# Kernel tuning notes

Measured on AMD Instinct MI355X. Metric: run time of the kernel, lower is better.

The kernel has to match this reference:

```python
import jax, jax.numpy as jnp
import numpy as np

B, N, DIM = 4, 1024, 2048
H, HKV, D = 16, 4, 128          # n_heads, n_kv_heads, head_dim
CACHE = 3072                     # cached KV length
WINDOW = 2048                    # max_window_len (sliding window)
EPS = 1e-6


def setup_inputs() -> dict:
    key = jax.random.key(0)
    ks = jax.random.split(key, 10)
    x = jax.random.normal(ks[0], (B, N, DIM), dtype=jnp.float32)
    past_k = jax.random.normal(ks[1], (B, HKV, CACHE, D), dtype=jnp.float32)
    past_v = jax.random.normal(ks[2], (B, HKV, CACHE, D), dtype=jnp.float32)
    # RoPE angles for the current segment (absolute positions CACHE..CACHE+N-1),
    # matching MultiLevelRoPE 'face' level: freqs = 1/theta**(arange(0,D,2)/D)
    pos = jnp.arange(CACHE, CACHE + N, dtype=jnp.float32)
    inv_freq = 1.0 / (10000.0 ** (jnp.arange(0, D, 2, dtype=jnp.float32) / D))
    ang = pos[:, None] * inv_freq[None, :]          # [N, D//2]
    freqs_cos = jnp.cos(ang)
    freqs_sin = jnp.sin(ang)
    s = 0.02
    Wq = jax.random.normal(ks[3], (H * D, DIM), dtype=jnp.float32) * s
    Wk = jax.random.normal(ks[4], (HKV * D, DIM), dtype=jnp.float32) * s
    Wv = jax.random.normal(ks[5], (HKV * D, DIM), dtype=jnp.float32) * s
    Wo = jax.random.normal(ks[6], (DIM, H * D), dtype=jnp.float32) * s
    bo = jnp.zeros((DIM,), dtype=jnp.float32)
    wq_norm = jnp.ones((D,), dtype=jnp.float32)
    wk_norm = jnp.ones((D,), dtype=jnp.float32)
    return {"x": x, "past_k": past_k, "past_v": past_v,
            "freqs_cos": freqs_cos, "freqs_sin": freqs_sin,
            "Wq": Wq, "Wk": Wk, "Wv": Wv, "Wo": Wo, "bo": bo,
            "wq_norm": wq_norm, "wk_norm": wk_norm}


def _rms_norm(t, w):
    # torch.nn.RMSNorm over head_dim
    return t * jax.lax.rsqrt(jnp.mean(t * t, axis=-1, keepdims=True) + EPS) * w


def _rope(t, cos, sin):
    # interleaved-pair complex rotation, as in MultiLevelRoPE.apply
    # t: [B, h, N, D]; cos/sin: [N, D//2]
    t2 = t.reshape(*t.shape[:-1], D // 2, 2)
    x0, x1 = t2[..., 0], t2[..., 1]
    c = cos[None, None, :, :]
    s = sin[None, None, :, :]
    r0 = x0 * c - x1 * s
    r1 = x0 * s + x1 * c
    return jnp.stack([r0, r1], axis=-1).reshape(t.shape)


def reference(x, past_k, past_v, freqs_cos, freqs_sin,
              Wq, Wk, Wv, Wo, bo, wq_norm, wk_norm):
    # projections -> [B, h, N, D]
    q = (x @ Wq.T).reshape(B, N, H, D).transpose(0, 2, 1, 3)
    k = (x @ Wk.T).reshape(B, N, HKV, D).transpose(0, 2, 1, 3)
    v = (x @ Wv.T).reshape(B, N, HKV, D).transpose(0, 2, 1, 3)
    # qk rms_norm on head_dim
    q = _rms_norm(q, wq_norm)
    k = _rms_norm(k, wk_norm)
    # RoPE on current segment (cached K already rotated)
    q = _rope(q, freqs_cos, freqs_sin)
    k = _rope(k, freqs_cos, freqs_sin)
    # append to cache -> M = CACHE + N
    k_all = jnp.concatenate([past_k, k], axis=2)   # [B, HKV, M, D]
    v_all = jnp.concatenate([past_v, v], axis=2)
    # repeat_kv for GQA
    n_rep = H // HKV
    k_rep = jnp.repeat(k_all, n_rep, axis=1)       # [B, H, M, D]
    v_rep = jnp.repeat(v_all, n_rep, axis=1)
    M = CACHE + N
    scale = 1.0 / jnp.sqrt(jnp.asarray(D, dtype=q.dtype))
    scores = jnp.einsum('bhnd,bhmd->bhnm', q, k_rep) * scale
    # causal + sliding-window mask over absolute positions
    qpos = jnp.arange(N) + CACHE                   # [N]
    kpos = jnp.arange(M)                           # [M]
    allowed = (kpos[None, :] <= qpos[:, None]) & (qpos[:, None] - kpos[None, :] < WINDOW)
    scores = jnp.where(allowed[None, None], scores, jnp.asarray(-1e30, dtype=scores.dtype))
    probs = jax.nn.softmax(scores, axis=-1)
    attn = jnp.einsum('bhnm,bhmd->bhnd', probs, v_rep)
    attn = attn.transpose(0, 2, 1, 3).reshape(B, N, H * D)
    return attn @ Wo.T + bo
```

## Files before the change

kernel.cpp:

```cpp
#include <hip/hip_runtime.h>
#include <hip/hip_bf16.h>
#include <stdint.h>

typedef unsigned short u16;
typedef unsigned int u32;
typedef __attribute__((ext_vector_type(8))) __bf16 bfrag;
typedef __attribute__((ext_vector_type(4))) float f32x4;
typedef __attribute__((ext_vector_type(16))) float f32x16;
typedef __attribute__((ext_vector_type(4))) unsigned short u16x4;

__device__ __forceinline__ u16 f2bf(float f){
  union { float f; u32 u; } v; v.f = f;
  u32 u = v.u;
  return (u16)((u + 0x7fffu + ((u >> 16) & 1u)) >> 16);
}

__device__ __forceinline__ u32 cvtpk(float a, float b){
  u32 r; asm("v_cvt_pk_bf16_f32 %0, %1, %2" : "=v"(r) : "v"(a), "v"(b)); return r;
}
__device__ __forceinline__ void swap32(u32 &a, u32 &b){
  asm volatile("v_permlane32_swap_b32 %0, %1" : "+v"(a), "+v"(b));
}

__device__ __forceinline__ void gload_lds16(const void* g, void* l){
  __builtin_amdgcn_global_load_lds(
      (__attribute__((address_space(1))) void*)(unsigned long long)g,
      (__attribute__((address_space(3))) void*)(u32)(unsigned long long)l,
      16, 0, 0);
}

__global__ void __launch_bounds__(256) k_cvt(const float* __restrict__ s, u16* __restrict__ d, int n4){
  int i = blockIdx.x*256 + threadIdx.x;
  if (i >= n4) return;
  float4 v = ((const float4*)s)[i];
  u16x4 o; o[0]=f2bf(v.x); o[1]=f2bf(v.y); o[2]=f2bf(v.z); o[3]=f2bf(v.w);
  ((u16x4*)d)[i] = o;
}

__global__ void __launch_bounds__(256) k_past_kr(const float* __restrict__ pk, u16* __restrict__ Kr){
  __shared__ u16 TK[64][128];
  const int kc = 16 + blockIdx.x;
  const int pl = blockIdx.y;
  const int t = threadIdx.x;
  const float* src = pk + (size_t)pl*393216 + (size_t)kc*8192;
  #pragma unroll
  for (int i = 0; i < 8; ++i){
    int e = i*1024 + t*4;
    float4 v = *(const float4*)(src + e);
    u16x4 o; o[0]=f2bf(v.x); o[1]=f2bf(v.y); o[2]=f2bf(v.z); o[3]=f2bf(v.w);
    *(u16x4*)&TK[e>>7][e&127] = o;
  }
  __syncthreads();
  u16* dst = Kr + (size_t)pl*524288 + (size_t)kc*8192;
  #pragma unroll
  for (int i = 0; i < 4; ++i){
    int f = i*256 + t;
    int fhi = f >> 6, lf = f & 63;
    int row = ((f >> 9) << 5) | (lf & 31);
    int col = ((fhi & 7) << 4) | ((lf >> 5) << 3);
    bfrag v = *(const bfrag*)&TK[row][col];
    *(bfrag*)(dst + fhi*512 + lf*8) = v;
  }
}

__global__ void __launch_bounds__(256) k_past_vr(const float* __restrict__ pv, u16* __restrict__ Vr){
  __shared__ u16 T2[128][80];
  const int kc = 16 + blockIdx.x;
  const int pl = blockIdx.y;
  const int t = threadIdx.x;
  const float* src = pv + (size_t)pl*393216 + (size_t)kc*8192;
  #pragma unroll
  for (int i = 0; i < 8; ++i){
    int e = i*1024 + t*4;
    int row = e >> 7, d0 = e & 127;
    float4 v = *(const float4*)(src + e);
    T2[d0][row]   = f2bf(v.x);
    T2[d0+1][row] = f2bf(v.y);
    T2[d0+2][row] = f2bf(v.z);
    T2[d0+3][row] = f2bf(v.w);
  }
  __syncthreads();
  u16* dst = Vr + (size_t)pl*524288 + (size_t)kc*8192;
  #pragma unroll
  for (int i = 0; i < 4; ++i){
    int g = i*256 + t;
    int ghi = g >> 6, lg = g & 63;
    int d  = ((ghi & 3) << 5) | (lg & 31);
    int k0 = ((g >> 9) << 5) | (((ghi >> 2) & 1) << 4) | ((lg >> 5) << 3);
    bfrag v = *(const bfrag*)&T2[d][k0];
    *(bfrag*)(dst + ghi*512 + lg*8) = v;
  }
}

__global__ void __launch_bounds__(256) k_new_vr(const u16* __restrict__ vn, u16* __restrict__ Vr){
  __shared__ u16 T2[128][80];
  const int kcl = blockIdx.x;
  const int pl = blockIdx.y;
  const int t = threadIdx.x;
  const u16* src = vn + (size_t)pl*131072 + (size_t)kcl*8192;
  #pragma unroll
  for (int i = 0; i < 4; ++i){
    int e = i*2048 + t*8;
    int row = e >> 7, d0 = e & 127;
    union { bfrag v; u16 x[8]; } u;
    u.v = *(const bfrag*)(src + e);
    #pragma unroll
    for (int j = 0; j < 8; ++j) T2[d0+j][row] = u.x[j];
  }
  __syncthreads();
  u16* dst = Vr + (size_t)pl*524288 + (size_t)(48 + kcl)*8192;
  #pragma unroll
  for (int i = 0; i < 4; ++i){
    int g = i*256 + t;
    int ghi = g >> 6, lg = g & 63;
    int d  = ((ghi & 3) << 5) | (lg & 31);
    int k0 = ((g >> 9) << 5) | (((ghi >> 2) & 1) << 4) | ((lg >> 5) << 3);
    bfrag v = *(const bfrag*)&T2[d][k0];
    *(bfrag*)(dst + ghi*512 + lg*8) = v;
  }
}

template<int EPI>
__global__ void __launch_bounds__(256) k_gemm(
    const u16* __restrict__ A, const u16* __restrict__ Bm,
    u16* __restrict__ Cb, float* __restrict__ Cf, const float* __restrict__ bias,
    int M, int Nn, int K)
{
  __shared__ u16 lsA[2][4096];
  __shared__ u16 lsB[2][4096];
  const int t = threadIdx.x, lane = t & 63, wid = t >> 6;
  const int l15 = lane & 15, l4 = lane >> 4;
  const int wm = wid >> 1, wn = wid & 1;
  const int bn = blockIdx.x, bm = blockIdx.y;
  const u16* Ab = A + (size_t)bm*128*K;
  const u16* Bb = Bm + (size_t)bn*128*K;

  auto stage = [&](u16* ls, const u16* g, int kof){
    #pragma unroll
    for (int r = 0; r < 2; ++r){
      int row = r*64 + (t >> 2);
      int s = (t & 3) ^ ((row >> 1) & 3);
      gload_lds16(g + (size_t)row*K + kof + s*8, ls + r*2048 + wid*512);
    }
  };

  f32x4 acc[4][4] = {};
  stage(&lsA[0][0], Ab, 0);
  stage(&lsB[0][0], Bb, 0);
  const int NT = K >> 5;
  const int sl = l4 ^ ((l15 >> 1) & 3);
  const int ra0 = wm*64 + l15, rb0 = wn*64 + l15;
  for (int kt = 0; kt < NT; ++kt){
    __syncthreads();
    const int cur = kt & 1;
    if (kt + 1 < NT){
      stage(&lsA[cur ^ 1][0], Ab, (kt + 1)*32);
      stage(&lsB[cur ^ 1][0], Bb, (kt + 1)*32);
    }
    bfrag af[4], bfv[4];
    #pragma unroll
    for (int i = 0; i < 4; ++i){
      af[i]  = *(const bfrag*)&lsA[cur][(ra0 + i*16)*32 + sl*8];
      bfv[i] = *(const bfrag*)&lsB[cur][(rb0 + i*16)*32 + sl*8];
    }
    #pragma unroll
    for (int i = 0; i < 4; ++i)
      #pragma unroll
      for (int j = 0; j < 4; ++j)
        acc[i][j] = __builtin_amdgcn_mfma_f32_16x16x32_bf16(af[i], bfv[j], acc[i][j], 0, 0, 0);
  }
  const int row0 = bm*128 + wm*64, col0 = bn*128 + wn*64;
  #pragma unroll
  for (int i = 0; i < 4; ++i)
    #pragma unroll
    for (int j = 0; j < 4; ++j){
      int cc = col0 + j*16 + l15;
      float bv = (EPI == 1) ? bias[cc] : 0.f;
      #pragma unroll
      for (int r = 0; r < 4; ++r){
        int rr = row0 + i*16 + l4*4 + r;
        if (EPI == 0) Cb[(size_t)rr*Nn + cc] = f2bf(acc[i][j][r]);
        else          Cf[(size_t)rr*Nn + cc] = acc[i][j][r] + bv;
      }
    }
}

__global__ void __launch_bounds__(256) k_rmsrope(
    const u16* __restrict__ proj, const float* __restrict__ cosb, const float* __restrict__ sinb,
    const float* __restrict__ wq, const float* __restrict__ wk,
    u16* __restrict__ q_ro, u16* __restrict__ Kr, u16* __restrict__ v_new)
{
  const int bn = blockIdx.x;
  const int b = bn >> 10, n = bn & 1023;
  const int lane = threadIdx.x & 63, w = threadIdx.x >> 6;
  const int chunk = blockIdx.y*4 + w;
  const u16* src = proj + (size_t)bn*3072 + chunk*128 + lane*2;
  const u32 raw = *(const u32*)src;
  union { u32 u; float f; } a, c2;
  a.u = raw << 16; c2.u = raw & 0xffff0000u;
  float x0 = a.f, x1 = c2.f;
  if (chunk >= 20){
    int hk = chunk - 20;
    *(u32*)(v_new + ((size_t)(b*4 + hk)*1024 + n)*128 + lane*2) = raw;
    return;
  }
  float ss = x0*x0 + x1*x1;
  #pragma unroll
  for (int m = 1; m < 64; m <<= 1) ss += __shfl_xor(ss, m, 64);
  float inv = rsqrtf(ss*(1.f/128.f) + 1e-6f);
  const float* wn2 = (chunk < 16) ? wq : wk;
  x0 *= inv*wn2[lane*2]; x1 *= inv*wn2[lane*2 + 1];
  float cz = cosb[n*64 + lane], sz = sinb[n*64 + lane];
  float r0 = x0*cz - x1*sz;
  float r1 = x0*sz + x1*cz;
  if (chunk < 16){
    const float KLF = 0.127529904f;
    r0 *= KLF; r1 *= KLF;
    u32 outp = (u32)f2bf(r0) | ((u32)f2bf(r1) << 16);
    *(u32*)(q_ro + (((size_t)(b*16 + chunk)*1024 + n) << 7) + lane*2) = outp;
  } else {
    int hk = chunk - 16;
    u32 outp = (u32)f2bf(r0) | ((u32)f2bf(r1) << 16);
    int kpos = 3072 + n;
    size_t idx = (size_t)(b*4 + hk)*524288
               + (size_t)(((kpos >> 6)*16) + (((kpos >> 5) & 1)*8) + (lane >> 3))*512
               + (size_t)((((lane >> 2) & 1) << 5) | (kpos & 31))*8
               + ((2*lane) & 7);
    *(u32*)(Kr + idx) = outp;
  }
}

__global__ void __launch_bounds__(512, 2) k_attn(
    const u16* __restrict__ q_ro, const u16* __restrict__ Kr,
    const u16* __restrict__ Vr, u16* __restrict__ attn_o)
{
  __shared__ u16 smem[32768];
  __shared__ float Lsh[4][32];
  const int bid = blockIdx.x;
  const int xcd = bid & 7, idx = bid >> 3;
  const int plane = (xcd << 1) | (idx >> 5);
  const int qt = idx & 31;
  const int b = plane >> 2, hk = plane & 3;
  const int t = threadIdx.x, lane = t & 63, w = t >> 6;
  const int l31 = lane & 31, lh = lane >> 5;
  const int hf = w >> 2;
  const int hd = w & 3;
  const int h = hk*4 + hd;
  const int qbase = qt*32;

  const u16* qplane = q_ro + (size_t)(b*16 + h)*1024*128;
  const u16* kplane = Kr + (size_t)(b*4 + hk)*524288;
  const u16* vplane = Vr + (size_t)(b*4 + hk)*524288;

  bfrag qf[8];
  {
    const u16* qrow = qplane + (size_t)(qbase + l31)*128 + lh*8;
    #pragma unroll
    for (int dks = 0; dks < 8; ++dks)
      qf[dks] = *(const bfrag*)(qrow + dks*16);
  }

  const int kb0 = (qbase + 1024) & ~63;
  const int kc0 = kb0 >> 6;
  const int qpos = 3072 + qbase + l31;

  const char* smb = (const char*)smem;
  const int krd = hf*8192 + lane*16;
  const int vrd = 32768 + hf*8192 + lane*16;

  auto stageK = [&](int c2, int buf){
    const u16* ks = kplane + (size_t)(kc0 + c2)*8192 + t*8;
    gload_lds16(ks,        smem + buf*8192 + t*8);
    gload_lds16(ks + 4096, smem + buf*8192 + 4096 + t*8);
  };
  auto stageV = [&](int c2, int buf){
    const u16* vs = vplane + (size_t)(kc0 + c2)*8192 + t*8;
    gload_lds16(vs,        smem + 16384 + buf*8192 + t*8);
    gload_lds16(vs + 4096, smem + 16384 + buf*8192 + 4096 + t*8);
  };

  f32x16 acc_o[4] = {};
  float l_run = 0.f;

  stageK(0, 0); stageK(1, 1); stageV(0, 0);
  __syncthreads();

  f32x16 sA, sB;
  {
    #pragma unroll
    for (int r = 0; r < 16; ++r) sA[r] = 0.f;
    __builtin_amdgcn_s_setprio(1);
    #pragma unroll
    for (int dks = 0; dks < 8; ++dks){
      bfrag kf = *(const bfrag*)(smb + krd + dks*1024);
      sA = __builtin_amdgcn_mfma_f32_32x32x16_bf16(kf, qf[dks], sA, 0, 0, 0);
    }
    __builtin_amdgcn_s_setprio(0);
  }

  auto body = [&](int c, f32x16& sCur, f32x16& sNxt){
    __syncthreads();
    if (c <= 30) stageK(c + 2, c & 1);
    if (c <= 31) stageV(c + 1, (c + 1) & 1);

    if (c < 32){
      #pragma unroll
      for (int r = 0; r < 16; ++r) sNxt[r] = 0.f;
      const int kbase = krd + ((c + 1) & 1)*16384;
      __builtin_amdgcn_s_setprio(1);
      #pragma unroll
      for (int dks = 0; dks < 8; ++dks){
        bfrag kf = *(const bfrag*)(smb + kbase + dks*1024);
        sNxt = __builtin_amdgcn_mfma_f32_32x32x16_bf16(kf, qf[dks], sNxt, 0, 0, 0);
      }
      __builtin_amdgcn_s_setprio(0);
    }

    bfrag vf[8];
    const int vbase = vrd + (c & 1)*16384;
    #pragma unroll
    for (int g = 0; g < 8; ++g) vf[g] = *(const bfrag*)(smb + vbase + g*1024);

    if ((c == 0) | (c == 32)){
      const int kb = kb0 + c*64;
      #pragma unroll
      for (int r = 0; r < 16; ++r){
        int kpos = kb + hf*32 + (r & 3) + 8*(r >> 2) + 4*lh;
        int dq = qpos - kpos;
        if ((unsigned)dq >= 2048u) sCur[r] = -1e30f;
      }
    }

    #pragma unroll
    for (int r = 0; r < 16; ++r) sCur[r] = exp2f(sCur[r]);
    {
      float a0 = (sCur[0]+sCur[1]) + (sCur[2]+sCur[3]);
      float a1 = (sCur[4]+sCur[5]) + (sCur[6]+sCur[7]);
      float a2 = (sCur[8]+sCur[9]) + (sCur[10]+sCur[11]);
      float a3 = (sCur[12]+sCur[13]) + (sCur[14]+sCur[15]);
      float lc = (a0 + a1) + (a2 + a3);
      lc += __shfl_xor(lc, 32, 64);
      l_run += lc;
    }

    union { u32 u[4]; bfrag v; } pf[2];
    {
      u32 a0 = cvtpk(sCur[0],  sCur[1]),  a1 = cvtpk(sCur[2],  sCur[3]);
      u32 b0 = cvtpk(sCur[4],  sCur[5]),  b1 = cvtpk(sCur[6],  sCur[7]);
      swap32(a0, b0); swap32(a1, b1);
      pf[0].u[0]=a0; pf[0].u[1]=a1; pf[0].u[2]=b0; pf[0].u[3]=b1;
      u32 c0 = cvtpk(sCur[8],  sCur[9]),  c1 = cvtpk(sCur[10], sCur[11]);
      u32 e0 = cvtpk(sCur[12], sCur[13]), e1 = cvtpk(sCur[14], sCur[15]);
      swap32(c0, e0); swap32(c1, e1);
      pf[1].u[0]=c0; pf[1].u[1]=c1; pf[1].u[2]=e0; pf[1].u[3]=e1;
    }

    __builtin_amdgcn_s_setprio(1);
    #pragma unroll
    for (int lks = 0; lks < 2; ++lks)
      #pragma unroll
      for (int dj = 0; dj < 4; ++dj)
        acc_o[dj] = __builtin_amdgcn_mfma_f32_32x32x16_bf16(vf[lks*4 + dj], pf[lks].v, acc_o[dj], 0, 0, 0);
    __builtin_amdgcn_s_setprio(0);
  };

  #pragma unroll 1
  for (int cc = 0; cc < 16; ++cc){
    body(2*cc,     sA, sB);
    body(2*cc + 1, sB, sA);
  }
  body(32, sA, sB);

  #pragma unroll
  for (int p = 0; p < 2; ++p){
    __syncthreads();
    if (hf == 1 && (hd >> 1) == p){
      if (lh == 0) Lsh[hd][l31] = l_run;
      float* om = (float*)smem + (hd & 1)*4096;
      #pragma unroll
      for (int dj = 0; dj < 4; ++dj)
        #pragma unroll
        for (int rg = 0; rg < 4; ++rg){
          int slot = dj*8 + rg*2 + lh;
          f32x4 vv;
          #pragma unroll
          for (int j = 0; j < 4; ++j) vv[j] = acc_o[dj][rg*4 + j];
          *(f32x4*)&om[l31*128 + ((slot ^ (l31 & 7)) << 2)] = vv;
        }
    }
    __syncthreads();
    if (hf == 0 && (hd >> 1) == p){
      const float* om = (const float*)smem + (hd & 1)*4096;
      float ltot = l_run + Lsh[hd][l31];
      float inv = 1.0f / ltot;
      const int bn = b*1024 + qbase + l31;
      u16* orow = attn_o + (size_t)bn*2048 + h*128;
      #pragma unroll
      for (int dj = 0; dj < 4; ++dj)
        #pragma unroll
        for (int rg = 0; rg < 4; ++rg){
          int slot = dj*8 + rg*2 + lh;
          f32x4 vv = *(const f32x4*)&om[l31*128 + ((slot ^ (l31 & 7)) << 2)];
          int d0 = dj*32 + rg*8 + lh*4;
          u16x4 o;
          #pragma unroll
          for (int j = 0; j < 4; ++j) o[j] = f2bf((acc_o[dj][rg*4 + j] + vv[j])*inv);
          *(u16x4*)(orow + d0) = o;
        }
    }
  }
}

extern "C" void kernel_launch(void* const* d_in, const int* in_sizes, int n_in,
                              void* d_out, int out_size, void* d_ws, size_t ws_size,
                              hipStream_t stream)
{
  const float* x      = (const float*)d_in[0];
  const float* past_k = (const float*)d_in[1];
  const float* past_v = (const float*)d_in[2];
  const float* fcos   = (const float*)d_in[3];
  const float* fsin   = (const float*)d_in[4];
  const float* Wq     = (const float*)d_in[5];
  const float* Wk     = (const float*)d_in[6];
  const float* Wv     = (const float*)d_in[7];
  const float* Wo     = (const float*)d_in[8];
  const float* bo     = (const float*)d_in[9];
  const float* wqn    = (const float*)d_in[10];
  const float* wkn    = (const float*)d_in[11];
  float* out = (float*)d_out;
  char* ws = (char*)d_ws;

  u16* xb    = (u16*)(ws);
  u16* wqkv  = (u16*)(ws + 16777216);
  u16* wo_b  = (u16*)(ws + 29360128);
  u16* q_ro  = (u16*)(ws + 37748736);
  u16* Kr    = (u16*)(ws + 54525952);
  u16* Vr    = (u16*)(ws + 71303168);
  u16* v_new = (u16*)(ws + 88080384);
  u16* proj  = (u16*)(ws + 92274688);
  u16* attn_o = proj;

  k_cvt<<<8192, 256, 0, stream>>>(x, xb, 2097152);
  k_cvt<<<4096, 256, 0, stream>>>(Wq, wqkv, 1048576);
  k_cvt<<<1024, 256, 0, stream>>>(Wk, wqkv + 2048*2048, 262144);
  k_cvt<<<1024, 256, 0, stream>>>(Wv, wqkv + 2560*2048, 262144);
  k_cvt<<<4096, 256, 0, stream>>>(Wo, wo_b, 1048576);
  k_past_kr<<<dim3(32, 16), 256, 0, stream>>>(past_k, Kr);
  k_past_vr<<<dim3(32, 16), 256, 0, stream>>>(past_v, Vr);

  k_gemm<0><<<dim3(24, 32), 256, 0, stream>>>(xb, wqkv, proj, nullptr, nullptr, 4096, 3072, 2048);
  k_rmsrope<<<dim3(4096, 6), 256, 0, stream>>>(proj, fcos, fsin, wqn, wkn, q_ro, Kr, v_new);
  k_new_vr<<<dim3(16, 16), 256, 0, stream>>>(v_new, Vr);
  k_attn<<<512, 512, 0, stream>>>(q_ro, Kr, Vr, attn_o);
  k_gemm<1><<<dim3(16, 32), 256, 0, stream>>>(attn_o, wo_b, nullptr, out, bo, 4096, 2048, 2048);
}
```

Measured before the change: 255.4 us.

## Pre-swizzle GEMM operands into MFMA fragment layout and enlarge GEMM tiles

```diff
diff --git a/kernel.cpp b/kernel.cpp
--- a/kernel.cpp
+++ b/kernel.cpp
@@ -29,12 +29,18 @@
       16, 0, 0);
 }
 
-__global__ void __launch_bounds__(256) k_cvt(const float* __restrict__ s, u16* __restrict__ d, int n4){
+__global__ void __launch_bounds__(256) k_cvt_frag(const float* __restrict__ s, u16* __restrict__ d,
+                                                  int n4, int NF, int n_off){
   int i = blockIdx.x*256 + threadIdx.x;
   if (i >= n4) return;
+  int e = i*4;
+  int ln = e >> 11, k = e & 2047;
+  int n = n_off + ln;
   float4 v = ((const float4*)s)[i];
   u16x4 o; o[0]=f2bf(v.x); o[1]=f2bf(v.y); o[2]=f2bf(v.z); o[3]=f2bf(v.w);
-  ((u16x4*)d)[i] = o;
+  size_t idx = ((size_t)((k >> 5)*NF + (n >> 4)))*512
+             + (size_t)(((n & 15) | (((k >> 3) & 3) << 4)))*8 + (k & 4);
+  *(u16x4*)(d + idx) = o;
 }
 
 __global__ void __launch_bounds__(256) k_past_kr(const float* __restrict__ pk, u16* __restrict__ Kr){
@@ -121,59 +127,50 @@
 }
 
 template<int EPI>
-__global__ void __launch_bounds__(256) k_gemm(
-    const u16* __restrict__ A, const u16* __restrict__ Bm,
-    u16* __restrict__ Cb, float* __restrict__ Cf, const float* __restrict__ bias,
-    int M, int Nn, int K)
+__global__ void __launch_bounds__(512, 2) k_gemm(
+    const u16* __restrict__ Af, const u16* __restrict__ Bf,
+    u16* __restrict__ Cb, float* __restrict__ Cf, const float* __restrict__ bias, int Nn)
 {
-  __shared__ u16 lsA[2][4096];
+  __shared__ u16 lsA[2][8192];
   __shared__ u16 lsB[2][4096];
-  const int t = threadIdx.x, lane = t & 63, wid = t >> 6;
+  const int t = threadIdx.x, lane = t & 63;
   const int l15 = lane & 15, l4 = lane >> 4;
-  const int wm = wid >> 1, wn = wid & 1;
+  const int w = t >> 6, wm = w >> 2, wn = w & 3;
   const int bn = blockIdx.x, bm = blockIdx.y;
-  const u16* Ab = A + (size_t)bm*128*K;
-  const u16* Bb = Bm + (size_t)bn*128*K;
-
-  auto stage = [&](u16* ls, const u16* g, int kof){
-    #pragma unroll
-    for (int r = 0; r < 2; ++r){
-      int row = r*64 + (t >> 2);
-      int s = (t & 3) ^ ((row >> 1) & 3);
-      gload_lds16(g + (size_t)row*K + kof + s*8, ls + r*2048 + wid*512);
-    }
-  };
-
-  f32x4 acc[4][4] = {};
-  stage(&lsA[0][0], Ab, 0);
-  stage(&lsB[0][0], Bb, 0);
-  const int NT = K >> 5;
-  const int sl = l4 ^ ((l15 >> 1) & 3);
-  const int ra0 = wm*64 + l15, rb0 = wn*64 + l15;
-  for (int kt = 0; kt < NT; ++kt){
+  const int NF = Nn >> 4;
+  const u16* As = Af + (size_t)(bm*16)*512 + t*8;
+
+  f32x4 acc[8][2] = {};
+  gload_lds16(As,        &lsA[0][t*8]);
+  gload_lds16(As + 4096, &lsA[0][4096 + t*8]);
+  gload_lds16(Bf + ((size_t)bn*8)*512 + t*8, &lsB[0][t*8]);
+
+  for (int kt = 0; kt < 64; ++kt){
     __syncthreads();
     const int cur = kt & 1;
-    if (kt + 1 < NT){
-      stage(&lsA[cur ^ 1][0], Ab, (kt + 1)*32);
-      stage(&lsB[cur ^ 1][0], Bb, (kt + 1)*32);
-    }
-    bfrag af[4], bfv[4];
-    #pragma unroll
-    for (int i = 0; i < 4; ++i){
-      af[i]  = *(const bfrag*)&lsA[cur][(ra0 + i*16)*32 + sl*8];
-      bfv[i] = *(const bfrag*)&lsB[cur][(rb0 + i*16)*32 + sl*8];
-    }
-    #pragma unroll
-    for (int i = 0; i < 4; ++i)
-      #pragma unroll
-      for (int j = 0; j < 4; ++j)
-        acc[i][j] = __builtin_amdgcn_mfma_f32_16x16x32_bf16(af[i], bfv[j], acc[i][j], 0, 0, 0);
-  }
-  const int row0 = bm*128 + wm*64, col0 = bn*128 + wn*64;
-  #pragma unroll
-  for (int i = 0; i < 4; ++i)
-    #pragma unroll
-    for (int j = 0; j < 4; ++j){
+    if (kt < 63){
+      const u16* An = As + (size_t)(kt + 1)*131072;
+      const u16* Bn = Bf + ((size_t)(kt + 1)*NF + bn*8)*512 + t*8;
+      gload_lds16(An,        &lsA[cur ^ 1][t*8]);
+      gload_lds16(An + 4096, &lsA[cur ^ 1][4096 + t*8]);
+      gload_lds16(Bn,        &lsB[cur ^ 1][t*8]);
+    }
+    bfrag bf2[2];
+    #pragma unroll
+    for (int j = 0; j < 2; ++j)
+      bf2[j] = *(const bfrag*)&lsB[cur][(wn*2 + j)*512 + lane*8];
+    #pragma unroll
+    for (int i = 0; i < 8; ++i){
+      bfrag af = *(const bfrag*)&lsA[cur][(wm*8 + i)*512 + lane*8];
+      acc[i][0] = __builtin_amdgcn_mfma_f32_16x16x32_bf16(af, bf2[0], acc[i][0], 0, 0, 0);
+      acc[i][1] = __builtin_amdgcn_mfma_f32_16x16x32_bf16(af, bf2[1], acc[i][1], 0, 0, 0);
+    }
+  }
+  const int row0 = bm*256 + wm*128, col0 = bn*128 + wn*32;
+  #pragma unroll
+  for (int i = 0; i < 8; ++i)
+    #pragma unroll
+    for (int j = 0; j < 2; ++j){
       int cc = col0 + j*16 + l15;
       float bv = (EPI == 1) ? bias[cc] : 0.f;
       #pragma unroll
@@ -232,7 +229,7 @@
 
 __global__ void __launch_bounds__(512, 2) k_attn(
     const u16* __restrict__ q_ro, const u16* __restrict__ Kr,
-    const u16* __restrict__ Vr, u16* __restrict__ attn_o)
+    const u16* __restrict__ Vr, u16* __restrict__ Aof)
 {
   __shared__ u16 smem[32768];
   __shared__ float Lsh[4][32];
@@ -287,15 +284,18 @@
 
   f32x16 sA, sB;
   {
-    #pragma unroll
-    for (int r = 0; r < 16; ++r) sA[r] = 0.f;
+    f32x16 p0 = {}, p1 = {};
     __builtin_amdgcn_s_setprio(1);
     #pragma unroll
-    for (int dks = 0; dks < 8; ++dks){
-      bfrag kf = *(const bfrag*)(smb + krd + dks*1024);
-      sA = __builtin_amdgcn_mfma_f32_32x32x16_bf16(kf, qf[dks], sA, 0, 0, 0);
+    for (int dks = 0; dks < 4; ++dks){
+      bfrag k0 = *(const bfrag*)(smb + krd + dks*1024);
+      bfrag k1 = *(const bfrag*)(smb + krd + (dks + 4)*1024);
+      p0 = __builtin_amdgcn_mfma_f32_32x32x16_bf16(k0, qf[dks], p0, 0, 0, 0);
+      p1 = __builtin_amdgcn_mfma_f32_32x32x16_bf16(k1, qf[dks + 4], p1, 0, 0, 0);
     }
     __builtin_amdgcn_s_setprio(0);
+    #pragma unroll
+    for (int r = 0; r < 16; ++r) sA[r] = p0[r] + p1[r];
   }
 
   auto body = [&](int c, f32x16& sCur, f32x16& sNxt){
@@ -304,16 +304,19 @@
     if (c <= 31) stageV(c + 1, (c + 1) & 1);
 
     if (c < 32){
-      #pragma unroll
-      for (int r = 0; r < 16; ++r) sNxt[r] = 0.f;
+      f32x16 p0 = {}, p1 = {};
       const int kbase = krd + ((c + 1) & 1)*16384;
       __builtin_amdgcn_s_setprio(1);
       #pragma unroll
-      for (int dks = 0; dks < 8; ++dks){
-        bfrag kf = *(const bfrag*)(smb + kbase + dks*1024);
-        sNxt = __builtin_amdgcn_mfma_f32_32x32x16_bf16(kf, qf[dks], sNxt, 0, 0, 0);
+      for (int dks = 0; dks < 4; ++dks){
+        bfrag k0 = *(const bfrag*)(smb + kbase + dks*1024);
+        bfrag k1 = *(const bfrag*)(smb + kbase + (dks + 4)*1024);
+        p0 = __builtin_amdgcn_mfma_f32_32x32x16_bf16(k0, qf[dks], p0, 0, 0, 0);
+        p1 = __builtin_amdgcn_mfma_f32_32x32x16_bf16(k1, qf[dks + 4], p1, 0, 0, 0);
       }
       __builtin_amdgcn_s_setprio(0);
+      #pragma unroll
+      for (int r = 0; r < 16; ++r) sNxt[r] = p0[r] + p1[r];
     }
 
     bfrag vf[8];
@@ -394,18 +397,17 @@
       float ltot = l_run + Lsh[hd][l31];
       float inv = 1.0f / ltot;
       const int bn = b*1024 + qbase + l31;
-      u16* orow = attn_o + (size_t)bn*2048 + h*128;
       #pragma unroll
       for (int dj = 0; dj < 4; ++dj)
         #pragma unroll
         for (int rg = 0; rg < 4; ++rg){
-          int slot = dj*8 + rg*2 + lh;
-          f32x4 vv = *(const f32x4*)&om[l31*128 + ((slot ^ (l31 & 7)) << 2)];
-          int d0 = dj*32 + rg*8 + lh*4;
+          f32x4 vv = *(const f32x4*)&om[l31*128 + (((dj*8 + rg*2 + lh) ^ (l31 & 7)) << 2)];
           u16x4 o;
           #pragma unroll
           for (int j = 0; j < 4; ++j) o[j] = f2bf((acc_o[dj][rg*4 + j] + vv[j])*inv);
-          *(u16x4*)(orow + d0) = o;
+          size_t idx = ((size_t)((h*4 + dj)*256 + (bn >> 4)))*512
+                     + (size_t)(((bn & 15) | (rg << 4)))*8 + lh*4;
+          *(u16x4*)(Aof + idx) = o;
         }
     }
   }
@@ -430,27 +432,27 @@
   float* out = (float*)d_out;
   char* ws = (char*)d_ws;
 
-  u16* xb    = (u16*)(ws);
-  u16* wqkv  = (u16*)(ws + 16777216);
-  u16* wo_b  = (u16*)(ws + 29360128);
+  u16* Axf   = (u16*)(ws);
+  u16* Wqkvf = (u16*)(ws + 16777216);
+  u16* Wof   = (u16*)(ws + 29360128);
   u16* q_ro  = (u16*)(ws + 37748736);
   u16* Kr    = (u16*)(ws + 54525952);
   u16* Vr    = (u16*)(ws + 71303168);
   u16* v_new = (u16*)(ws + 88080384);
   u16* proj  = (u16*)(ws + 92274688);
-  u16* attn_o = proj;
-
-  k_cvt<<<8192, 256, 0, stream>>>(x, xb, 2097152);
-  k_cvt<<<4096, 256, 0, stream>>>(Wq, wqkv, 1048576);
-  k_cvt<<<1024, 256, 0, stream>>>(Wk, wqkv + 2048*2048, 262144);
-  k_cvt<<<1024, 256, 0, stream>>>(Wv, wqkv + 2560*2048, 262144);
-  k_cvt<<<4096, 256, 0, stream>>>(Wo, wo_b, 1048576);
+  u16* Aof   = proj;
+
+  k_cvt_frag<<<8192, 256, 0, stream>>>(x,  Axf, 2097152, 256, 0);
+  k_cvt_frag<<<4096, 256, 0, stream>>>(Wq, Wqkvf, 1048576, 192, 0);
+  k_cvt_frag<<<1024, 256, 0, stream>>>(Wk, Wqkvf, 262144, 192, 2048);
+  k_cvt_frag<<<1024, 256, 0, stream>>>(Wv, Wqkvf, 262144, 192, 2560);
+  k_cvt_frag<<<4096, 256, 0, stream>>>(Wo, Wof, 1048576, 128, 0);
   k_past_kr<<<dim3(32, 16), 256, 0, stream>>>(past_k, Kr);
   k_past_vr<<<dim3(32, 16), 256, 0, stream>>>(past_v, Vr);
 
-  k_gemm<0><<<dim3(24, 32), 256, 0, stream>>>(xb, wqkv, proj, nullptr, nullptr, 4096, 3072, 2048);
+  k_gemm<0><<<dim3(24, 16), 512, 0, stream>>>(Axf, Wqkvf, proj, nullptr, nullptr, 3072);
   k_rmsrope<<<dim3(4096, 6), 256, 0, stream>>>(proj, fcos, fsin, wqn, wkn, q_ro, Kr, v_new);
   k_new_vr<<<dim3(16, 16), 256, 0, stream>>>(v_new, Vr);
-  k_attn<<<512, 512, 0, stream>>>(q_ro, Kr, Vr, attn_o);
-  k_gemm<1><<<dim3(16, 32), 256, 0, stream>>>(attn_o, wo_b, nullptr, out, bo, 4096, 2048, 2048);
-}
+  k_attn<<<512, 512, 0, stream>>>(q_ro, Kr, Vr, Aof);
+  k_gemm<1><<<dim3(16, 16), 512, 0, stream>>>(Aof, Wof, nullptr, out, bo, 2048);
+}
```

Measured after the change: 275.5 us. 1.08x slower.

## Software-pipeline PV MFMA one chunk behind with triple-buffered V

Applied to the files above, without the earlier changes.

```diff
diff --git a/kernel.cpp b/kernel.cpp
--- a/kernel.cpp
+++ b/kernel.cpp
@@ -230,11 +230,11 @@
   }
 }
 
-__global__ void __launch_bounds__(512, 2) k_attn(
+__global__ void __launch_bounds__(512, 1) k_attn(
     const u16* __restrict__ q_ro, const u16* __restrict__ Kr,
     const u16* __restrict__ Vr, u16* __restrict__ attn_o)
 {
-  __shared__ u16 smem[32768];
+  __shared__ u16 smem[40960];
   __shared__ float Lsh[4][32];
   const int bid = blockIdx.x;
   const int xcd = bid & 7, idx = bid >> 3;
@@ -273,53 +273,70 @@
     gload_lds16(ks,        smem + buf*8192 + t*8);
     gload_lds16(ks + 4096, smem + buf*8192 + 4096 + t*8);
   };
-  auto stageV = [&](int c2, int buf){
+  auto stageV = [&](int c2, int slot){
     const u16* vs = vplane + (size_t)(kc0 + c2)*8192 + t*8;
-    gload_lds16(vs,        smem + 16384 + buf*8192 + t*8);
-    gload_lds16(vs + 4096, smem + 16384 + buf*8192 + 4096 + t*8);
+    gload_lds16(vs,        smem + 16384 + slot*8192 + t*8);
+    gload_lds16(vs + 4096, smem + 16384 + slot*8192 + 4096 + t*8);
   };
 
   f32x16 acc_o[4] = {};
   float l_run = 0.f;
+  union pfu { u32 u[4]; bfrag v; };
+  pfu pf0, pf1;
 
   stageK(0, 0); stageK(1, 1); stageV(0, 0);
   __syncthreads();
 
   f32x16 sA, sB;
   {
-    #pragma unroll
-    for (int r = 0; r < 16; ++r) sA[r] = 0.f;
+    f32x16 p0 = {}, p1 = {};
     __builtin_amdgcn_s_setprio(1);
     #pragma unroll
-    for (int dks = 0; dks < 8; ++dks){
-      bfrag kf = *(const bfrag*)(smb + krd + dks*1024);
-      sA = __builtin_amdgcn_mfma_f32_32x32x16_bf16(kf, qf[dks], sA, 0, 0, 0);
+    for (int dks = 0; dks < 4; ++dks){
+      bfrag k0 = *(const bfrag*)(smb + krd + dks*1024);
+      bfrag k1 = *(const bfrag*)(smb + krd + (dks + 4)*1024);
+      p0 = __builtin_amdgcn_mfma_f32_32x32x16_bf16(k0, qf[dks], p0, 0, 0, 0);
+      p1 = __builtin_amdgcn_mfma_f32_32x32x16_bf16(k1, qf[dks + 4], p1, 0, 0, 0);
     }
     __builtin_amdgcn_s_setprio(0);
+    #pragma unroll
+    for (int r = 0; r < 16; ++r) sA[r] = p0[r] + p1[r];
   }
 
   auto body = [&](int c, f32x16& sCur, f32x16& sNxt){
     __syncthreads();
     if (c <= 30) stageK(c + 2, c & 1);
-    if (c <= 31) stageV(c + 1, (c + 1) & 1);
-
+    if (c <= 31) stageV(c + 1, (c + 1) % 3);
+
+    __builtin_amdgcn_s_setprio(1);
     if (c < 32){
-      #pragma unroll
-      for (int r = 0; r < 16; ++r) sNxt[r] = 0.f;
+      f32x16 p0 = {}, p1 = {};
       const int kbase = krd + ((c + 1) & 1)*16384;
-      __builtin_amdgcn_s_setprio(1);
-      #pragma unroll
-      for (int dks = 0; dks < 8; ++dks){
-        bfrag kf = *(const bfrag*)(smb + kbase + dks*1024);
-        sNxt = __builtin_amdgcn_mfma_f32_32x32x16_bf16(kf, qf[dks], sNxt, 0, 0, 0);
+      #pragma unroll
+      for (int dks = 0; dks < 4; ++dks){
+        bfrag k0 = *(const bfrag*)(smb + kbase + dks*1024);
+        bfrag k1 = *(const bfrag*)(smb + kbase + (dks + 4)*1024);
+        p0 = __builtin_amdgcn_mfma_f32_32x32x16_bf16(k0, qf[dks], p0, 0, 0, 0);
+        p1 = __builtin_amdgcn_mfma_f32_32x32x16_bf16(k1, qf[dks + 4], p1, 0, 0, 0);
       }
-      __builtin_amdgcn_s_setprio(0);
-    }
-
-    bfrag vf[8];
-    const int vbase = vrd + (c & 1)*16384;
-    #pragma unroll
-    for (int g = 0; g < 8; ++g) vf[g] = *(const bfrag*)(smb + vbase + g*1024);
+      #pragma unroll
+      for (int r = 0; r < 16; ++r) sNxt[r] = p0[r] + p1[r];
+    }
+
+    if (c > 0){
+      const int vbase = vrd + ((c - 1) % 3)*16384;
+      #pragma unroll
+      for (int dj = 0; dj < 4; ++dj){
+        bfrag vf = *(const bfrag*)(smb + vbase + dj*1024);
+        acc_o[dj] = __builtin_amdgcn_mfma_f32_32x32x16_bf16(vf, pf0.v, acc_o[dj], 0, 0, 0);
+      }
+      #pragma unroll
+      for (int dj = 0; dj < 4; ++dj){
+        bfrag vf = *(const bfrag*)(smb + vbase + (4 + dj)*1024);
+        acc_o[dj] = __builtin_amdgcn_mfma_f32_32x32x16_bf16(vf, pf1.v, acc_o[dj], 0, 0, 0);
+      }
+    }
+    __builtin_amdgcn_s_setprio(0);
 
     if ((c == 0) | (c == 32)){
       const int kb = kb0 + c*64;
@@ -342,26 +359,16 @@
       lc += __shfl_xor(lc, 32, 64);
       l_run += lc;
     }
-
-    union { u32 u[4]; bfrag v; } pf[2];
     {
       u32 a0 = cvtpk(sCur[0],  sCur[1]),  a1 = cvtpk(sCur[2],  sCur[3]);
       u32 b0 = cvtpk(sCur[4],  sCur[5]),  b1 = cvtpk(sCur[6],  sCur[7]);
       swap32(a0, b0); swap32(a1, b1);
-      pf[0].u[0]=a0; pf[0].u[1]=a1; pf[0].u[2]=b0; pf[0].u[3]=b1;
+      pf0.u[0]=a0; pf0.u[1]=a1; pf0.u[2]=b0; pf0.u[3]=b1;
       u32 c0 = cvtpk(sCur[8],  sCur[9]),  c1 = cvtpk(sCur[10], sCur[11]);
       u32 e0 = cvtpk(sCur[12], sCur[13]), e1 = cvtpk(sCur[14], sCur[15]);
       swap32(c0, e0); swap32(c1, e1);
-      pf[1].u[0]=c0; pf[1].u[1]=c1; pf[1].u[2]=e0; pf[1].u[3]=e1;
-    }
-
-    __builtin_amdgcn_s_setprio(1);
-    #pragma unroll
-    for (int lks = 0; lks < 2; ++lks)
-      #pragma unroll
-      for (int dj = 0; dj < 4; ++dj)
-        acc_o[dj] = __builtin_amdgcn_mfma_f32_32x32x16_bf16(vf[lks*4 + dj], pf[lks].v, acc_o[dj], 0, 0, 0);
-    __builtin_amdgcn_s_setprio(0);
+      pf1.u[0]=c0; pf1.u[1]=c1; pf1.u[2]=e0; pf1.u[3]=e1;
+    }
   };
 
   #pragma unroll 1
@@ -370,6 +377,22 @@
     body(2*cc + 1, sB, sA);
   }
   body(32, sA, sB);
+
+  {
+    const int vbase = vrd + 2*16384;
+    __builtin_amdgcn_s_setprio(1);
+    #pragma unroll
+    for (int dj = 0; dj < 4; ++dj){
+      bfrag vf = *(const bfrag*)(smb + vbase + dj*1024);
+      acc_o[dj] = __builtin_amdgcn_mfma_f32_32x32x16_bf16(vf, pf0.v, acc_o[dj], 0, 0, 0);
+    }
+    #pragma unroll
+    for (int dj = 0; dj < 4; ++dj){
+      bfrag vf = *(const bfrag*)(smb + vbase + (4 + dj)*1024);
+      acc_o[dj] = __builtin_amdgcn_mfma_f32_32x32x16_bf16(vf, pf1.v, acc_o[dj], 0, 0, 0);
+    }
+    __builtin_amdgcn_s_setprio(0);
+  }
 
   #pragma unroll
   for (int p = 0; p < 2; ++p){
```

New measurement: 257.8 us. No clear change (+0.9%).
